# Kernel tuning notes

Hardware: AMD Instinct MI355X
Metric: run time of the kernel (lower is better)

## Reference

```python
import jax, jax.numpy as jnp
import numpy as np

B_SZ, SEQ = 16, 2048
VOCAB, EMBED = 50257, 128
DSTATE, HID, NCLS = 16, 256, 10
NEDGE = 8192  # edges per graph (avg degree 4)
LN_EPS = 1e-5


def setup_inputs() -> dict:
    key = jax.random.key(0)
    ks = jax.random.split(key, 12)
    tokens = jax.random.randint(ks[0], (B_SZ, SEQ), 0, VOCAB, dtype=jnp.int32)
    lengths = jnp.full((B_SZ,), SEQ, dtype=jnp.int32)  # full-length graphs
    edge_indices = jax.random.randint(ks[1], (B_SZ, 2, NEDGE), 0, SEQ, dtype=jnp.int32)
    emb = (jax.random.normal(ks[2], (VOCAB, EMBED)) * 0.02).at[0].set(0.0)  # padding_idx=0
    A_log = jax.random.normal(ks[3], (EMBED, DSTATE)) * 0.1
    B_w = jax.random.normal(ks[4], (DSTATE, EMBED)) * (1.0 / np.sqrt(EMBED))
    C_w = jax.random.normal(ks[5], (EMBED, DSTATE)) * (1.0 / np.sqrt(DSTATE))
    D_skip = jnp.ones((EMBED,))
    ln_g = jnp.ones((EMBED,))
    ln_b = jnp.zeros((EMBED,))
    Wmsg_w = jax.random.normal(ks[6], (HID, EMBED)) * (1.0 / np.sqrt(EMBED))
    Wupd_w = jax.random.normal(ks[7], (HID, EMBED + HID)) * (1.0 / np.sqrt(EMBED + HID))
    Wupd_b = jax.random.normal(ks[8], (HID,)) * 0.01
    cls_w = jax.random.normal(ks[9], (NCLS, HID)) * (1.0 / np.sqrt(HID))
    cls_b = jnp.zeros((NCLS,))
    return {"tokens": tokens, "lengths": lengths, "edge_indices": edge_indices,
            "emb": emb, "A_log": A_log, "B_w": B_w, "C_w": C_w, "D_skip": D_skip,
            "ln_g": ln_g, "ln_b": ln_b, "Wmsg_w": Wmsg_w, "Wupd_w": Wupd_w,
            "Wupd_b": Wupd_b, "cls_w": cls_w, "cls_b": cls_b}


def _ssm(x, A_log, B_w, C_w, D_skip, ln_g, ln_b):
    # x: (B, S, d_model). Diagonal SSM: h_t = h_{t-1}*exp(A) + B x_t (broadcast over d_model)
    Aexp = jnp.exp(-jnp.exp(A_log))  # (d_model, d_state)
    h0 = jnp.zeros((x.shape[0], EMBED, DSTATE), dtype=x.dtype)

    def step(h, x_t):  # x_t: (B, d_model)
        b_t = x_t @ B_w.T                            # (B, d_state)
        h = h * Aexp[None] + b_t[:, None, :]          # (B, d_model, d_state)
        y = h.mean(axis=1) @ C_w.T + D_skip * x_t     # (B, d_model)
        return h, y

    _, ys = jax.lax.scan(step, h0, jnp.swapaxes(x, 0, 1))
    out = jnp.swapaxes(ys, 0, 1)                      # (B, S, d_model)
    mu = out.mean(-1, keepdims=True)
    var = jnp.mean((out - mu) ** 2, axis=-1, keepdims=True)
    return ln_g * (out - mu) * jax.lax.rsqrt(var + LN_EPS) + ln_b


def reference(tokens, lengths, edge_indices, emb, A_log, B_w, C_w, D_skip,
              ln_g, ln_b, Wmsg_w, Wupd_w, Wupd_b, cls_w, cls_b):
    x = emb[tokens]                                   # (B, S, E)
    h = _ssm(x, A_log, B_w, C_w, D_skip, ln_g, ln_b)  # (B, S, E)
    src, dst = edge_indices[:, 0, :], edge_indices[:, 1, :]   # (B, Ne)
    h_src = jnp.take_along_axis(h, src[:, :, None], axis=1)   # (B, Ne, E)
    msgs = jnp.einsum('bed,hd->beh', h_src, Wmsg_w)            # (B, Ne, H)
    flat_dst = (jnp.arange(B_SZ, dtype=dst.dtype)[:, None] * SEQ + dst).reshape(-1)
    agg = jax.ops.segment_sum(msgs.reshape(-1, HID), flat_dst,
                              num_segments=B_SZ * SEQ).reshape(B_SZ, SEQ, HID)
    upd = jax.nn.relu(jnp.concatenate([h, agg], axis=-1) @ Wupd_w.T + Wupd_b)  # (B, S, H)
    pooled = upd.mean(axis=1)                          # (B, H)  (all lengths == SEQ)
    return pooled @ cls_w.T + cls_b                    # (B, NCLS)
```

## Files before the change

kernel.cpp:

```cpp
#include <hip/hip_runtime.h>

#define B_SZ   16
#define SEQ    2048
#define VOCAB  50257
#define EMBED  128
#define DSTATE 16
#define HID    256
#define NCLS   10
#define NEDGE  8192
#define KTR    64
#define LN_EPS 1e-5f
#define NROW   (B_SZ*SEQ)
#define BCAP   32
#define OVCAP  1024

#define PB_CAST   4096
#define PB_BUCKET (PB_CAST + 512)
#define PB_PRECM  (PB_BUCKET + 128)
#define PB_CTAB   (PB_PRECM + 16)
#define PB_PRECB  (PB_CTAB + 1)
#define PB_TOTAL  (PB_PRECB + 1)

typedef float  f32x4 __attribute__((ext_vector_type(4)));
typedef short  s16x8 __attribute__((ext_vector_type(8)));

__device__ __forceinline__ float scrub(float x){
  return (x == x && fabsf(x) < 1e30f) ? x : 0.f;
}
__device__ __forceinline__ short f2b(float f){
  unsigned int u = __float_as_uint(f);
  unsigned int r = (u + 0x7fffu + ((u >> 16) & 1u)) >> 16;
  return (short)r;
}
__device__ __forceinline__ unsigned int pack2(float a, float b){
  return (unsigned int)(unsigned short)f2b(a)
       | ((unsigned int)(unsigned short)f2b(b) << 16);
}
__device__ __forceinline__ float lo2f(unsigned int v){ return __uint_as_float(v << 16); }
__device__ __forceinline__ float hi2f(unsigned int v){ return __uint_as_float(v & 0xffff0000u); }

__global__ __launch_bounds__(256) void k_prep(
    const int* __restrict__ tokens, const float* __restrict__ emb,
    const float* __restrict__ A_log, const float* __restrict__ B_w,
    const float* __restrict__ Wmsg, const float* __restrict__ Wupd,
    const int* __restrict__ edges, const float* __restrict__ cls_b,
    float* __restrict__ c_tab, short* __restrict__ Bf, float* __restrict__ MT,
    unsigned int* __restrict__ x_bf, int* __restrict__ cnt,
    unsigned short* __restrict__ bucket, int* __restrict__ ovf_cnt,
    int* __restrict__ ovf, float* __restrict__ out){
  int bid = blockIdx.x, tid = threadIdx.x;
  if (bid < PB_CAST){
    int gid = bid*256 + tid;
    int row = gid >> 5, ch = gid & 31;
    int tok = tokens[row];
    tok = tok < 0 ? 0 : (tok >= VOCAB ? VOCAB-1 : tok);
    float4 v = *(const float4*)(emb + (size_t)tok*EMBED + ch*4);
    uint2 o; o.x = pack2(v.x, v.y); o.y = pack2(v.z, v.w);
    *(uint2*)(x_bf + (size_t)row*(EMBED/2) + ch*2) = o;
  } else if (bid < PB_BUCKET){
    int eid = (bid-PB_CAST)*256 + tid;
    int b = eid >> 13, i = eid & (NEDGE-1);
    const int* ei = edges + (size_t)b*2*NEDGE;
    int s = ei[i]         & (SEQ-1);
    int d = ei[NEDGE + i] & (SEQ-1);
    int gdst = (b << 11) | d;
    int slot = atomicAdd(&cnt[gdst], 1);
    if (slot < BCAP) bucket[(size_t)gdst*BCAP + slot] = (unsigned short)s;
    else {
      int o = atomicAdd(ovf_cnt, 1);
      if (o < OVCAP) ovf[o] = ((b << 11) | s) | (gdst << 16);
    }
  } else if (bid < PB_PRECM){
    int hp = (bid-PB_BUCKET)*2 + (tid >> 7);
    int e  = tid & 127;
    const float* w2 = Wupd + (size_t)hp*384 + 128;
    float acc = 0.f;
    for (int h1 = 0; h1 < HID; ++h1)
      acc += Wmsg[h1*EMBED + e] * w2[h1];
    MT[(size_t)hp*EMBED + e] = scrub(acc);
  } else if (bid < PB_CTAB){
    if (tid < 64){
      int d = bid - PB_PRECM, lane = tid;
      float a0 = scrub(expf(-expf(A_log[(2*lane+0)*DSTATE + d])));
      float a1 = scrub(expf(-expf(A_log[(2*lane+1)*DSTATE + d])));
      float p0 = 1.f, p1 = 1.f;
      for (int k = 0; k < KTR; ++k){
        float s = p0 + p1;
        for (int off = 32; off; off >>= 1) s += __shfl_down(s, off);
        if (lane == 0) c_tab[k*DSTATE + d] = scrub(s * (1.0f/128.0f));
        p0 *= a0; p1 *= a1;
      }
    }
  } else if (bid < PB_PRECB){
    int idx = tid;
    int c = idx >> 6, lane = idx & 63;
    int n = lane & 15;
    int kb = c*32 + (lane >> 4)*8;
    short v[8];
    #pragma unroll
    for (int jj = 0; jj < 8; ++jj) v[jj] = f2b(B_w[(size_t)n*EMBED + kb + jj]);
    *(s16x8*)(Bf + (size_t)idx*8) = *(s16x8*)v;
  } else {
    if (tid < B_SZ*NCLS) out[tid] = cls_b[tid % NCLS];
  }
}

__global__ __launch_bounds__(256) void k_ssm_fused(
    const short* __restrict__ x_bf, const float* __restrict__ c_tab,
    const float* __restrict__ C_w, const float* __restrict__ D_skip,
    const float* __restrict__ ln_g, const float* __restrict__ ln_b,
    const short* __restrict__ Bf, const float* __restrict__ Wupd,
    const float* __restrict__ MT, unsigned int* __restrict__ h_out,
    short* __restrict__ Wcs){
  __shared__ float bsh[128][18];
  __shared__ float msh[64][18];
  __shared__ float Ct[DSTATE][EMBED+2];
  __shared__ float csh[KTR][DSTATE];
  int bid = blockIdx.x, tid = threadIdx.x;

  if (bid >= 512){
    int idx = (bid-512)*256 + tid;
    int c    = idx >> 10;
    int rem  = idx & 1023;
    int j    = rem >> 6;
    int lane = rem & 63;
    int n  = j*16 + (lane & 15);
    int kb = c*32 + (lane >> 4)*8;
    short v[8];
    #pragma unroll
    for (int jj = 0; jj < 8; ++jj){
      int k = kb + jj;
      float val = (k < 128) ? Wupd[(size_t)n*384 + k] : MT[(size_t)n*EMBED + (k-128)];
      v[jj] = f2b(val);
    }
    *(s16x8*)(Wcs + (size_t)idx*8) = *(s16x8*)v;
    return;
  }

  int b  = bid >> 5;
  int t0 = (bid & 31) * 64;
  for (int i = tid; i < DSTATE*EMBED; i += 256){
    int e = i >> 4, d = i & 15;
    Ct[d][e] = C_w[i];
  }
  for (int i = tid; i < KTR*DSTATE; i += 256)
    csh[i >> 4][i & 15] = c_tab[i];

  int wv = tid >> 6, lane = tid & 63;
  int m = lane & 15, lg = lane >> 4;

  const s16x8* Bp = (const s16x8*)Bf;
  #pragma unroll
  for (int tt = 0; tt < 2; ++tt){
    int tile = wv*2 + tt;
    int trow = t0 - 64 + tile*16;
    f32x4 acc = (f32x4){0.f,0.f,0.f,0.f};
    if (trow >= 0){
      const short* xrow = x_bf + ((size_t)(b*SEQ + trow + m))*EMBED + lg*8;
      #pragma unroll
      for (int c = 0; c < 4; ++c){
        s16x8 a = *(const s16x8*)(xrow + c*32);
        acc = __builtin_amdgcn_mfma_f32_16x16x32_bf16(a, Bp[c*64 + lane], acc, 0, 0, 0);
      }
    }
    #pragma unroll
    for (int r = 0; r < 4; ++r)
      bsh[tile*16 + lg*4 + r][m] = scrub(acc[r]);
  }
  __syncthreads();

  {
    int d = tid & 15;
    #pragma unroll
    for (int it = 0; it < 4; ++it){
      int q = (tid + it*256) >> 4;
      int t = t0 + q;
      int base = 64 + q;
      int kmax = (t+1 < KTR) ? t+1 : KTR;
      float acc = 0.f;
      for (int k = 0; k < kmax; ++k) acc += csh[k][d] * bsh[base-k][d];
      msh[q][d] = scrub(acc);
    }
  }
  __syncthreads();

  int e0 = lane*2;
  float2 dsk = *(const float2*)&D_skip[e0];
  float2 lgv = *(const float2*)&ln_g[e0];
  float2 lbv = *(const float2*)&ln_b[e0];
  const unsigned int* xb = (const unsigned int*)x_bf;
  for (int q = wv*16; q < wv*16+16; ++q){
    int row = b*SEQ + t0 + q;
    unsigned int xp = xb[(size_t)row*(EMBED/2) + lane];
    float x0 = lo2f(xp), x1 = hi2f(xp);
    float y0 = dsk.x*x0, y1 = dsk.y*x1;
    #pragma unroll
    for (int d = 0; d < DSTATE; ++d){
      float md = msh[q][d];
      y0 += md * Ct[d][e0];
      y1 += md * Ct[d][e0+1];
    }
    y0 = scrub(y0); y1 = scrub(y1);
    float s = y0+y1, s2 = y0*y0 + y1*y1;
    for (int off = 32; off; off >>= 1){ s += __shfl_down(s,off); s2 += __shfl_down(s2,off); }
    s = __shfl(s, 0); s2 = __shfl(s2, 0);
    float mu  = s * (1.f/EMBED);
    float var = s2 * (1.f/EMBED) - mu*mu;
    float inv = rsqrtf(fmaxf(var, 0.f) + LN_EPS);
    float o0 = scrub(lgv.x*(y0-mu)*inv + lbv.x);
    float o1 = scrub(lgv.y*(y1-mu)*inv + lbv.y);
    h_out[(size_t)row*(EMBED/2) + lane] = pack2(o0, o1);
  }
}

__global__ __launch_bounds__(256) void k_gather(
    const int* __restrict__ cnt, const unsigned short* __restrict__ bucket,
    const int* __restrict__ ovf_cnt, const int* __restrict__ ovf,
    const unsigned int* __restrict__ h, unsigned int* __restrict__ g){
  int wv = threadIdx.x >> 6, lane = threadIdx.x & 63;
  int gdst = blockIdx.x*4 + wv;
  int n = cnt[gdst]; n = n > BCAP ? BCAP : n;
  int b = gdst >> 11;
  const unsigned int* hb = h + (size_t)b*SEQ*(EMBED/2);
  const unsigned short* bk = bucket + (size_t)gdst*BCAP;
  float ax = 0.f, ay = 0.f;
  for (int i = 0; i < n; ++i){
    unsigned int v = hb[(size_t)bk[i]*(EMBED/2) + lane];
    ax += lo2f(v); ay += hi2f(v);
  }
  int on = *ovf_cnt; on = on > OVCAP ? OVCAP : on;
  for (int idx = 0; idx < on; ++idx){
    int pk = ovf[idx];
    if (((pk >> 16) & 0x7fff) == gdst){
      unsigned int v = h[(size_t)(pk & 0xffff)*(EMBED/2) + lane];
      ax += lo2f(v); ay += hi2f(v);
    }
  }
  g[(size_t)gdst*(EMBED/2) + lane] = pack2(scrub(ax), scrub(ay));
}

__global__ __launch_bounds__(256) void k_upd_mfma(
    const short* __restrict__ h, const short* __restrict__ g,
    const short* __restrict__ Wcs, const float* __restrict__ Wupd_b,
    const float* __restrict__ cls_w, float* __restrict__ out){
  __shared__ float psum[4*HID];
  __shared__ float clsw[NCLS*HID];
  int tid = threadIdx.x;
  int wave = blockIdx.x*4 + (tid >> 6);
  int lane = tid & 63;
  int row0 = wave * 16;
  int b = (blockIdx.x*64) >> 11;
  int m = lane & 15, lg = lane >> 4;
  const short* hrow = h + (size_t)(row0+m)*EMBED + lg*8;
  const short* grow = g + (size_t)(row0+m)*EMBED + lg*8;

  for (int i = tid; i < NCLS*HID; i += 256) clsw[i] = cls_w[i];

  f32x4 acc[16];
  #pragma unroll
  for (int j = 0; j < 16; ++j) acc[j] = (f32x4){0.f,0.f,0.f,0.f};

  const s16x8* Bp = (const s16x8*)Wcs;
  #pragma unroll
  for (int c = 0; c < 8; ++c){
    s16x8 a = (c < 4) ? *(const s16x8*)(hrow + c*32)
                      : *(const s16x8*)(grow + (c-4)*32);
    #pragma unroll
    for (int j = 0; j < 16; ++j){
      s16x8 bfr = Bp[(c*16 + j)*64 + lane];
      acc[j] = __builtin_amdgcn_mfma_f32_16x16x32_bf16(a, bfr, acc[j], 0, 0, 0);
    }
  }

  int wv = tid >> 6;
  #pragma unroll
  for (int j = 0; j < 16; ++j){
    int n = j*16 + (lane & 15);
    float bias = Wupd_b[n];
    float v = 0.f;
    #pragma unroll
    for (int r = 0; r < 4; ++r) v += fmaxf(acc[j][r] + bias, 0.f);
    v += __shfl_down(v, 32);
    v += __shfl_down(v, 16);
    if (lane < 16) psum[wv*HID + n] = scrub(v);
  }
  __syncthreads();
  float bp = psum[tid] + psum[HID+tid] + psum[2*HID+tid] + psum[3*HID+tid];
  psum[tid] = bp;
  __syncthreads();
  if (tid < 64){
    for (int c = 0; c < NCLS; ++c){
      float s = 0.f;
      #pragma unroll
      for (int k = 0; k < 4; ++k)
        s += psum[tid + k*64] * clsw[c*HID + tid + k*64];
      for (int off = 32; off; off >>= 1) s += __shfl_down(s, off);
      if (tid == 0) atomicAdd(&out[b*NCLS + c], scrub(s * (1.0f/SEQ)));
    }
  }
}

extern "C" void kernel_launch(void* const* d_in, const int* in_sizes, int n_in,
                              void* d_out, int out_size, void* d_ws, size_t ws_size,
                              hipStream_t stream) {
  const int*   tokens = (const int*)d_in[0];
  const int*   edges  = (const int*)d_in[2];
  const float* emb    = (const float*)d_in[3];
  const float* A_log  = (const float*)d_in[4];
  const float* B_w    = (const float*)d_in[5];
  const float* C_w    = (const float*)d_in[6];
  const float* D_skip = (const float*)d_in[7];
  const float* ln_g   = (const float*)d_in[8];
  const float* ln_b   = (const float*)d_in[9];
  const float* Wmsg   = (const float*)d_in[10];
  const float* Wupd   = (const float*)d_in[11];
  const float* Wupd_b = (const float*)d_in[12];
  const float* cls_w  = (const float*)d_in[13];
  const float* cls_b  = (const float*)d_in[14];
  float* out = (float*)d_out;

  char* ws = (char*)d_ws;
  float* c_tab = (float*)ws;  ws += 16*1024;
  float* MT    = (float*)ws;  ws += (size_t)HID*EMBED*4;
  short* Wcs   = (short*)ws;  ws += (size_t)HID*HID*2;
  short* Bf    = (short*)ws;  ws += 16*1024;
  char*  zbase = ws;
  int*   cnt   = (int*)ws;    ws += (size_t)NROW*4;
  int*   ovf_cnt = (int*)ws;  ws += 64;
  int*   ovf   = (int*)ws;    ws += OVCAP*4;
  size_t zlen = (size_t)((char*)ws - zbase);
  unsigned short* bucket = (unsigned short*)ws; ws += (size_t)NROW*BCAP*2;
  short* x_bf  = (short*)ws;  ws += (size_t)NROW*EMBED*2;
  short* h_bf  = (short*)ws;  ws += (size_t)NROW*EMBED*2;
  short* g_bf  = (short*)ws;  ws += (size_t)NROW*EMBED*2;

  hipMemsetAsync(zbase, 0, zlen, stream);
  hipLaunchKernelGGL(k_prep, dim3(PB_TOTAL), dim3(256), 0, stream,
                     tokens, emb, A_log, B_w, Wmsg, Wupd, edges, cls_b,
                     c_tab, Bf, MT, (unsigned int*)x_bf, cnt, bucket,
                     ovf_cnt, ovf, out);
  hipLaunchKernelGGL(k_ssm_fused, dim3(544), dim3(256), 0, stream,
                     x_bf, c_tab, C_w, D_skip, ln_g, ln_b, Bf, Wupd, MT,
                     (unsigned int*)h_bf, Wcs);
  hipLaunchKernelGGL(k_gather, dim3(NROW/4), dim3(256), 0, stream,
                     cnt, bucket, ovf_cnt, ovf, (const unsigned int*)h_bf,
                     (unsigned int*)g_bf);
  hipLaunchKernelGGL(k_upd_mfma, dim3(NROW/64), dim3(256), 0, stream,
                     h_bf, g_bf, Wcs, Wupd_b, cls_w, out);
}
```

Measured before the change: 194.4 us.

## Halve per-block work in SSM and update kernels to double grid parallelism

The SSM kernel now processes 32 timesteps per block instead of 64, doubling its grid to 1024 compute blocks plus the weight-cast blocks. The update GEMM kernel splits each 16-row group's 256 output columns across two waves, so each block covers 32 rows and the grid doubles, with fewer accumulator registers per wave. The aim is more blocks and waves to fill the GPU's many CUs and better hide latency. In exchange, the 64-step history prefix is recomputed for twice as many blocks, constant tables are loaded twice as often, and the A fragments are loaded redundantly by both waves.

```diff
diff --git a/kernel.cpp b/kernel.cpp
--- a/kernel.cpp
+++ b/kernel.cpp
@@ -13,6 +13,7 @@
 #define NROW   (B_SZ*SEQ)
 #define BCAP   32
 #define OVCAP  1024
+#define TT     32
 
 #define PB_CAST   4096
 #define PB_BUCKET (PB_CAST + 512)
@@ -112,14 +113,14 @@
     const short* __restrict__ Bf, const float* __restrict__ Wupd,
     const float* __restrict__ MT, unsigned int* __restrict__ h_out,
     short* __restrict__ Wcs){
-  __shared__ float bsh[128][18];
-  __shared__ float msh[64][18];
+  __shared__ float bsh[KTR+TT][18];
+  __shared__ float msh[TT][18];
   __shared__ float Ct[DSTATE][EMBED+2];
   __shared__ float csh[KTR][DSTATE];
   int bid = blockIdx.x, tid = threadIdx.x;
 
-  if (bid >= 512){
-    int idx = (bid-512)*256 + tid;
+  if (bid >= 1024){
+    int idx = (bid-1024)*256 + tid;
     int c    = idx >> 10;
     int rem  = idx & 1023;
     int j    = rem >> 6;
@@ -137,8 +138,8 @@
     return;
   }
 
-  int b  = bid >> 5;
-  int t0 = (bid & 31) * 64;
+  int b  = bid >> 6;
+  int t0 = (bid & 63) * TT;
   for (int i = tid; i < DSTATE*EMBED; i += 256){
     int e = i >> 4, d = i & 15;
     Ct[d][e] = C_w[i];
@@ -152,30 +153,32 @@
   const s16x8* Bp = (const s16x8*)Bf;
   #pragma unroll
   for (int tt = 0; tt < 2; ++tt){
-    int tile = wv*2 + tt;
-    int trow = t0 - 64 + tile*16;
-    f32x4 acc = (f32x4){0.f,0.f,0.f,0.f};
-    if (trow >= 0){
-      const short* xrow = x_bf + ((size_t)(b*SEQ + trow + m))*EMBED + lg*8;
+    int tile = wv + tt*4;
+    if (tile < 6){
+      int trow = t0 - KTR + tile*16;
+      f32x4 acc = (f32x4){0.f,0.f,0.f,0.f};
+      if (trow >= 0){
+        const short* xrow = x_bf + ((size_t)(b*SEQ + trow + m))*EMBED + lg*8;
+        #pragma unroll
+        for (int c = 0; c < 4; ++c){
+          s16x8 a = *(const s16x8*)(xrow + c*32);
+          acc = __builtin_amdgcn_mfma_f32_16x16x32_bf16(a, Bp[c*64 + lane], acc, 0, 0, 0);
+        }
+      }
       #pragma unroll
-      for (int c = 0; c < 4; ++c){
-        s16x8 a = *(const s16x8*)(xrow + c*32);
-        acc = __builtin_amdgcn_mfma_f32_16x16x32_bf16(a, Bp[c*64 + lane], acc, 0, 0, 0);
-      }
-    }
-    #pragma unroll
-    for (int r = 0; r < 4; ++r)
-      bsh[tile*16 + lg*4 + r][m] = scrub(acc[r]);
+      for (int r = 0; r < 4; ++r)
+        bsh[tile*16 + lg*4 + r][m] = scrub(acc[r]);
+    }
   }
   __syncthreads();
 
   {
     int d = tid & 15;
     #pragma unroll
-    for (int it = 0; it < 4; ++it){
+    for (int it = 0; it < 2; ++it){
       int q = (tid + it*256) >> 4;
       int t = t0 + q;
-      int base = 64 + q;
+      int base = KTR + q;
       int kmax = (t+1 < KTR) ? t+1 : KTR;
       float acc = 0.f;
       for (int k = 0; k < kmax; ++k) acc += csh[k][d] * bsh[base-k][d];
@@ -189,7 +192,7 @@
   float2 lgv = *(const float2*)&ln_g[e0];
   float2 lbv = *(const float2*)&ln_b[e0];
   const unsigned int* xb = (const unsigned int*)x_bf;
-  for (int q = wv*16; q < wv*16+16; ++q){
+  for (int q = wv*8; q < wv*8+8; ++q){
     int row = b*SEQ + t0 + q;
     unsigned int xp = xb[(size_t)row*(EMBED/2) + lane];
     float x0 = lo2f(xp), x1 = hi2f(xp);
@@ -246,19 +249,23 @@
   __shared__ float psum[4*HID];
   __shared__ float clsw[NCLS*HID];
   int tid = threadIdx.x;
-  int wave = blockIdx.x*4 + (tid >> 6);
-  int lane = tid & 63;
-  int row0 = wave * 16;
-  int b = (blockIdx.x*64) >> 11;
+  #pragma unroll
+  for (int i = 0; i < 4; ++i) psum[tid + i*256] = 0.f;
+  for (int i = tid; i < NCLS*HID; i += 256) clsw[i] = cls_w[i];
+  __syncthreads();
+
+  int wv = tid >> 6, lane = tid & 63;
+  int rg = blockIdx.x*2 + (wv >> 1);
+  int ch = wv & 1;
+  int row0 = rg * 16;
+  int b = (blockIdx.x*32) >> 11;
   int m = lane & 15, lg = lane >> 4;
   const short* hrow = h + (size_t)(row0+m)*EMBED + lg*8;
   const short* grow = g + (size_t)(row0+m)*EMBED + lg*8;
 
-  for (int i = tid; i < NCLS*HID; i += 256) clsw[i] = cls_w[i];
-
-  f32x4 acc[16];
-  #pragma unroll
-  for (int j = 0; j < 16; ++j) acc[j] = (f32x4){0.f,0.f,0.f,0.f};
+  f32x4 acc[8];
+  #pragma unroll
+  for (int j = 0; j < 8; ++j) acc[j] = (f32x4){0.f,0.f,0.f,0.f};
 
   const s16x8* Bp = (const s16x8*)Wcs;
   #pragma unroll
@@ -266,16 +273,16 @@
     s16x8 a = (c < 4) ? *(const s16x8*)(hrow + c*32)
                       : *(const s16x8*)(grow + (c-4)*32);
     #pragma unroll
-    for (int j = 0; j < 16; ++j){
-      s16x8 bfr = Bp[(c*16 + j)*64 + lane];
+    for (int j = 0; j < 8; ++j){
+      int jj = ch*8 + j;
+      s16x8 bfr = Bp[(c*16 + jj)*64 + lane];
       acc[j] = __builtin_amdgcn_mfma_f32_16x16x32_bf16(a, bfr, acc[j], 0, 0, 0);
     }
   }
 
-  int wv = tid >> 6;
-  #pragma unroll
-  for (int j = 0; j < 16; ++j){
-    int n = j*16 + (lane & 15);
+  #pragma unroll
+  for (int j = 0; j < 8; ++j){
+    int n = (ch*8 + j)*16 + (lane & 15);
     float bias = Wupd_b[n];
     float v = 0.f;
     #pragma unroll
@@ -339,12 +346,12 @@
                      tokens, emb, A_log, B_w, Wmsg, Wupd, edges, cls_b,
                      c_tab, Bf, MT, (unsigned int*)x_bf, cnt, bucket,
                      ovf_cnt, ovf, out);
-  hipLaunchKernelGGL(k_ssm_fused, dim3(544), dim3(256), 0, stream,
+  hipLaunchKernelGGL(k_ssm_fused, dim3(1056), dim3(256), 0, stream,
                      x_bf, c_tab, C_w, D_skip, ln_g, ln_b, Bf, Wupd, MT,
                      (unsigned int*)h_bf, Wcs);
   hipLaunchKernelGGL(k_gather, dim3(NROW/4), dim3(256), 0, stream,
                      cnt, bucket, ovf_cnt, ovf, (const unsigned int*)h_bf,
                      (unsigned int*)g_bf);
-  hipLaunchKernelGGL(k_upd_mfma, dim3(NROW/64), dim3(256), 0, stream,
+  hipLaunchKernelGGL(k_upd_mfma, dim3(NROW/32), dim3(256), 0, stream,
                      h_bf, g_bf, Wcs, Wupd_b, cls_w, out);
 }
```

New measurement: 205.7 us. 5.8% more time.

## Fuse neighbor gather into MFMA update kernel via shared-memory staging

Applied to the files above, without the earlier changes.

Merges the gather kernel into the update/MFMA kernel. Each block now gathers neighbor sums for its 64 rows into padded shared memory, then reads the g operand from LDS instead of a global g buffer. This drops one launch and the global write and re-read of g. In exchange the gather loses parallelism: only 512 blocks each loop serially over 16 rows per wave, where there were 8192 blocks before, so latency hiding for the irregular loads may suffer.

```diff
diff --git a/kernel.cpp b/kernel.cpp
--- a/kernel.cpp
+++ b/kernel.cpp
@@ -13,6 +13,7 @@
 #define NROW   (B_SZ*SEQ)
 #define BCAP   32
 #define OVCAP  1024
+#define GROWS  136
 
 #define PB_CAST   4096
 #define PB_BUCKET (PB_CAST + 512)
@@ -213,48 +214,50 @@
   }
 }
 
-__global__ __launch_bounds__(256) void k_gather(
-    const int* __restrict__ cnt, const unsigned short* __restrict__ bucket,
+__global__ __launch_bounds__(256) void k_gupd(
+    const short* __restrict__ h, const int* __restrict__ cnt,
+    const unsigned short* __restrict__ bucket,
     const int* __restrict__ ovf_cnt, const int* __restrict__ ovf,
-    const unsigned int* __restrict__ h, unsigned int* __restrict__ g){
-  int wv = threadIdx.x >> 6, lane = threadIdx.x & 63;
-  int gdst = blockIdx.x*4 + wv;
-  int n = cnt[gdst]; n = n > BCAP ? BCAP : n;
-  int b = gdst >> 11;
-  const unsigned int* hb = h + (size_t)b*SEQ*(EMBED/2);
-  const unsigned short* bk = bucket + (size_t)gdst*BCAP;
-  float ax = 0.f, ay = 0.f;
-  for (int i = 0; i < n; ++i){
-    unsigned int v = hb[(size_t)bk[i]*(EMBED/2) + lane];
-    ax += lo2f(v); ay += hi2f(v);
-  }
-  int on = *ovf_cnt; on = on > OVCAP ? OVCAP : on;
-  for (int idx = 0; idx < on; ++idx){
-    int pk = ovf[idx];
-    if (((pk >> 16) & 0x7fff) == gdst){
-      unsigned int v = h[(size_t)(pk & 0xffff)*(EMBED/2) + lane];
-      ax += lo2f(v); ay += hi2f(v);
-    }
-  }
-  g[(size_t)gdst*(EMBED/2) + lane] = pack2(scrub(ax), scrub(ay));
-}
-
-__global__ __launch_bounds__(256) void k_upd_mfma(
-    const short* __restrict__ h, const short* __restrict__ g,
     const short* __restrict__ Wcs, const float* __restrict__ Wupd_b,
     const float* __restrict__ cls_w, float* __restrict__ out){
+  __shared__ short gsh[64*GROWS];
   __shared__ float psum[4*HID];
   __shared__ float clsw[NCLS*HID];
   int tid = threadIdx.x;
-  int wave = blockIdx.x*4 + (tid >> 6);
-  int lane = tid & 63;
-  int row0 = wave * 16;
-  int b = (blockIdx.x*64) >> 11;
+  int row0 = blockIdx.x * 64;
+  int b = row0 >> 11;
+  int wv = tid >> 6, lane = tid & 63;
+
+  for (int i = tid; i < NCLS*HID; i += 256) clsw[i] = cls_w[i];
+
+  {
+    unsigned int* gu = (unsigned int*)gsh;
+    const unsigned int* hb = (const unsigned int*)h + (size_t)b*SEQ*(EMBED/2);
+    int on = *ovf_cnt; on = on > OVCAP ? OVCAP : on;
+    for (int q = wv*16; q < wv*16+16; ++q){
+      int gdst = row0 + q;
+      int n = cnt[gdst]; n = n > BCAP ? BCAP : n;
+      const unsigned short* bk = bucket + (size_t)gdst*BCAP;
+      float ax = 0.f, ay = 0.f;
+      for (int i = 0; i < n; ++i){
+        unsigned int v = hb[(size_t)bk[i]*(EMBED/2) + lane];
+        ax += lo2f(v); ay += hi2f(v);
+      }
+      for (int idx = 0; idx < on; ++idx){
+        int pk = ovf[idx];
+        if (((pk >> 16) & 0x7fff) == gdst){
+          unsigned int v = ((const unsigned int*)h)[(size_t)(pk & 0xffff)*(EMBED/2) + lane];
+          ax += lo2f(v); ay += hi2f(v);
+        }
+      }
+      gu[q*(GROWS/2) + lane] = pack2(scrub(ax), scrub(ay));
+    }
+  }
+  __syncthreads();
+
   int m = lane & 15, lg = lane >> 4;
-  const short* hrow = h + (size_t)(row0+m)*EMBED + lg*8;
-  const short* grow = g + (size_t)(row0+m)*EMBED + lg*8;
-
-  for (int i = tid; i < NCLS*HID; i += 256) clsw[i] = cls_w[i];
+  const short* hrow = h + (size_t)(row0 + wv*16 + m)*EMBED + lg*8;
+  const short* grow = &gsh[(wv*16 + m)*GROWS + lg*8];
 
   f32x4 acc[16];
   #pragma unroll
@@ -272,7 +275,6 @@
     }
   }
 
-  int wv = tid >> 6;
   #pragma unroll
   for (int j = 0; j < 16; ++j){
     int n = j*16 + (lane & 15);
@@ -332,7 +334,6 @@
   unsigned short* bucket = (unsigned short*)ws; ws += (size_t)NROW*BCAP*2;
   short* x_bf  = (short*)ws;  ws += (size_t)NROW*EMBED*2;
   short* h_bf  = (short*)ws;  ws += (size_t)NROW*EMBED*2;
-  short* g_bf  = (short*)ws;  ws += (size_t)NROW*EMBED*2;
 
   hipMemsetAsync(zbase, 0, zlen, stream);
   hipLaunchKernelGGL(k_prep, dim3(PB_TOTAL), dim3(256), 0, stream,
@@ -342,9 +343,7 @@
   hipLaunchKernelGGL(k_ssm_fused, dim3(544), dim3(256), 0, stream,
                      x_bf, c_tab, C_w, D_skip, ln_g, ln_b, Bf, Wupd, MT,
                      (unsigned int*)h_bf, Wcs);
-  hipLaunchKernelGGL(k_gather, dim3(NROW/4), dim3(256), 0, stream,
-                     cnt, bucket, ovf_cnt, ovf, (const unsigned int*)h_bf,
-                     (unsigned int*)g_bf);
-  hipLaunchKernelGGL(k_upd_mfma, dim3(NROW/64), dim3(256), 0, stream,
-                     h_bf, g_bf, Wcs, Wupd_b, cls_w, out);
-}
+  hipLaunchKernelGGL(k_gupd, dim3(NROW/64), dim3(256), 0, stream,
+                     h_bf, cnt, bucket, ovf_cnt, ovf, Wcs, Wupd_b,
+                     cls_w, out);
+}
```

After: 211.6 us. +8.9%, slower.
